# Kernel tuning notes

Measured on AMD Instinct MI355X. Metric: run time of the kernel, lower is better.

Reference implementation:

```python
import jax, jax.numpy as jnp
import numpy as np

NEG_SLOPE = 0.2

def symlog(v):
    return jnp.sign(v) * jnp.log1p(jnp.abs(v))

def conv1d(v, w, b):
    # v: (N, Cin, L), w: (Cout, Cin, 3), 'same' padding, stride 1
    out = jax.lax.conv_general_dilated(v, w, (1,), 'SAME',
                                       dimension_numbers=('NCH', 'OIH', 'NCH'))
    return out + b[None, :, None]

def glorot(key, shape, fan_in, fan_out):
    s = jnp.sqrt(6.0 / (fan_in + fan_out))
    return jax.random.uniform(key, shape, jnp.float32, -s, s)

def setup_inputs() -> dict:
    N, L, E = 20000, 128, 320000
    IN, H, C, OHC = 512, 8, 32, 8
    key = jax.random.key(0)
    ks = jax.random.split(key, 12)
    x = jax.random.normal(ks[0], (N, IN), jnp.float32)
    onehot = jax.random.uniform(ks[1], (N, L), jnp.float32)
    src = jax.random.randint(ks[2], (E,), 0, N)
    off = jax.random.randint(ks[3], (E,), 1, N)
    dst = (src + off) % N  # guarantees no self loops
    adj = jnp.stack([src, dst], axis=0).astype(jnp.int64)
    lin_w = glorot(ks[4], (IN + OHC, H * C), IN + OHC, H * C)
    att_l = glorot(ks[5], (1, H, C), C, C)
    att_r = glorot(ks[6], (1, H, C), C, C)
    bias = jnp.zeros((H * C,), jnp.float32)
    conv1_w = glorot(ks[7], (8, 1, 3), 3, 24)
    conv1_b = jnp.zeros((8,), jnp.float32)
    conv2_w = glorot(ks[8], (16, 8, 3), 24, 48)
    conv2_b = jnp.zeros((16,), jnp.float32)
    lin2_w = glorot(ks[9], (16, OHC), 16, OHC)
    lin2_b = jnp.zeros((OHC,), jnp.float32)
    return {"x": x, "onehot": onehot, "adj": adj, "n_nodes": N,
            "lin_w": lin_w, "att_l": att_l, "att_r": att_r, "bias": bias,
            "conv1_w": conv1_w, "conv1_b": conv1_b,
            "conv2_w": conv2_w, "conv2_b": conv2_b,
            "lin2_w": lin2_w, "lin2_b": lin2_b}

def reference(x, onehot, adj, n_nodes, lin_w, att_l, att_r, bias,
              conv1_w, conv1_b, conv2_w, conv2_b, lin2_w, lin2_b):
    N = n_nodes
    H, C = att_l.shape[1], att_l.shape[2]
    # one-hot conv pipe: sort -> symlog -> conv-relu x2 -> global avg pool -> linear
    prepared = symlog(jnp.sort(onehot, axis=-1))[:, None, :]  # (N,1,L)
    h = jax.nn.relu(conv1d(prepared, conv1_w, conv1_b))
    h = jax.nn.relu(conv1d(h, conv2_w, conv2_b))
    readout = h.mean(axis=-1) @ lin2_w + lin2_b  # (N, OHC)
    xin = jnp.concatenate([x, readout], axis=-1)
    xh = (xin @ lin_w).reshape(N, H, C)
    al = (xh * att_l).sum(axis=-1)  # (N,H) sending alphas
    ar = (xh * att_r).sum(axis=-1)  # (N,H) receiving alphas
    # add self loops (input adj has none, so remove_self_loops is a no-op)
    loops = jnp.arange(N, dtype=adj.dtype)
    src = jnp.concatenate([adj[0], loops])
    dst = jnp.concatenate([adj[1], loops])
    # GAT-style attention with segment softmax over receiving nodes
    alpha = jax.nn.leaky_relu(al[src] + ar[dst], NEG_SLOPE)  # (Etot,H)
    amax = jax.ops.segment_max(alpha, dst, num_segments=N)
    ex = jnp.exp(alpha - amax[dst])
    denom = jax.ops.segment_sum(ex, dst, num_segments=N)
    alpha = ex / denom[dst]
    # weight + scatter-add aggregate
    wx = xh[src] * alpha[..., None]  # (Etot,H,C)
    new_x = jax.ops.segment_sum(wx, dst, num_segments=N).reshape(N, H * C) + bias
    new_onehot = jax.ops.segment_sum(onehot[src], dst, num_segments=N) + onehot
    return new_x, new_onehot
```

## Files before the change

### kernel.cpp

```cpp
#include <hip/hip_runtime.h>

#define NEG_SLOPE 0.2f

typedef __attribute__((ext_vector_type(4))) float f32x4;
typedef __attribute__((ext_vector_type(2))) float f32x2;
typedef __attribute__((ext_vector_type(8))) short short8;

__device__ __forceinline__ f32x2 mk2(float a, float b) { f32x2 r; r[0] = a; r[1] = b; return r; }

__device__ __forceinline__ f32x2 FMA2(f32x2 a, f32x2 b, f32x2 c) {
#if __has_builtin(__builtin_elementwise_fma)
    return __builtin_elementwise_fma(a, b, c);
#else
    f32x2 r; r[0] = fmaf(a[0], b[0], c[0]); r[1] = fmaf(a[1], b[1], c[1]); return r;
#endif
}

__device__ __forceinline__ ushort f2bf(float f) {
    uint u = __float_as_uint(f);
    u += 0x7FFFu + ((u >> 16) & 1u);
    return (ushort)(u >> 16);
}
__device__ __forceinline__ float bflo(uint u) { return __uint_as_float(u << 16); }
__device__ __forceinline__ float bfhi(uint u) { return __uint_as_float(u & 0xffff0000u); }

__global__ __launch_bounds__(256) void k_zero_int(int* __restrict__ p, int n) {
    int i = blockIdx.x * 256 + threadIdx.x;
    if (i < n) p[i] = 0;
}

__global__ __launch_bounds__(256) void k_conv_wave(
    const float* __restrict__ onehot,
    const float* __restrict__ c1w, const float* __restrict__ c1b,
    const float* __restrict__ c2w, const float* __restrict__ c2b,
    const float* __restrict__ l2w, const float* __restrict__ l2b,
    float* __restrict__ readout, uint* __restrict__ ohb, int N) {
    const int wave = threadIdx.x >> 6;
    const int lane = threadIdx.x & 63;
    const int n = blockIdx.x * 4 + wave;
    if (n >= N) return;

    float2 in2 = *reinterpret_cast<const float2*>(&onehot[(size_t)n * 128 + lane * 2]);
    ohb[(size_t)n*64 + lane] = (uint)f2bf(in2.x) | ((uint)f2bf(in2.y) << 16);
    float v0 = log1pf(in2.x);
    float v1 = log1pf(in2.y);

    #pragma unroll
    for (int k = 2; k <= 128; k <<= 1) {
        const bool asc = ((lane & (k >> 1)) == 0);
        #pragma unroll
        for (int j = k >> 1; j >= 2; j >>= 1) {
            const int m = j >> 1;
            float p0 = __shfl_xor(v0, m, 64);
            float p1 = __shfl_xor(v1, m, 64);
            const bool keepmin = (((lane & m) == 0) == asc);
            v0 = keepmin ? fminf(v0, p0) : fmaxf(v0, p0);
            v1 = keepmin ? fminf(v1, p1) : fmaxf(v1, p1);
        }
        float lo = fminf(v0, v1), hi = fmaxf(v0, v1);
        v0 = asc ? lo : hi;
        v1 = asc ? hi : lo;
    }

    float pm = __shfl_up(v1, 1, 64); if (lane == 0)  pm = 0.f;
    float pp = __shfl_down(v0, 1, 64); if (lane == 63) pp = 0.f;

    float h0[8], h1[8];
    {
        const f32x2 xm = mk2(pm, v0), x0 = mk2(v0, v1), xp = mk2(v1, pp);
        #pragma unroll
        for (int c = 0; c < 8; ++c) {
            const float w0 = c1w[c*3+0], w1 = c1w[c*3+1], w2 = c1w[c*3+2], b = c1b[c];
            f32x2 h = FMA2(xm, mk2(w0, w0), FMA2(x0, mk2(w1, w1), FMA2(xp, mk2(w2, w2), mk2(b, b))));
            h0[c] = fmaxf(h[0], 0.f);
            h1[c] = fmaxf(h[1], 0.f);
        }
    }

    f32x2 a01[16];
    #pragma unroll
    for (int c = 0; c < 16; ++c) { float b = c2b[c]; a01[c] = mk2(b, b); }
    #pragma unroll
    for (int ci = 0; ci < 8; ++ci) {
        float hm = __shfl_up(h1[ci], 1, 64); if (lane == 0)  hm = 0.f;
        float hp = __shfl_down(h0[ci], 1, 64); if (lane == 63) hp = 0.f;
        const f32x2 xm = mk2(hm, h0[ci]), x0 = mk2(h0[ci], h1[ci]), xp = mk2(h1[ci], hp);
        #pragma unroll
        for (int c = 0; c < 16; ++c) {
            const float w0 = c2w[(c*8+ci)*3+0], w1 = c2w[(c*8+ci)*3+1], w2 = c2w[(c*8+ci)*3+2];
            a01[c] = FMA2(xm, mk2(w0, w0), FMA2(x0, mk2(w1, w1), FMA2(xp, mk2(w2, w2), a01[c])));
        }
    }

    float pv[16];
    #pragma unroll
    for (int c = 0; c < 16; ++c) pv[c] = fmaxf(a01[c][0], 0.f) + fmaxf(a01[c][1], 0.f);

    {
        const bool up1 = lane & 1;
        #pragma unroll
        for (int j = 0; j < 8; ++j) {
            float send = up1 ? pv[j] : pv[j+8];
            float keep = up1 ? pv[j+8] : pv[j];
            pv[j] = keep + __shfl_xor(send, 1, 64);
        }
        const bool up2 = (lane >> 1) & 1;
        #pragma unroll
        for (int j = 0; j < 4; ++j) {
            float send = up2 ? pv[j] : pv[j+4];
            float keep = up2 ? pv[j+4] : pv[j];
            pv[j] = keep + __shfl_xor(send, 2, 64);
        }
        const bool up3 = (lane >> 2) & 1;
        #pragma unroll
        for (int j = 0; j < 2; ++j) {
            float send = up3 ? pv[j] : pv[j+2];
            float keep = up3 ? pv[j+2] : pv[j];
            pv[j] = keep + __shfl_xor(send, 4, 64);
        }
        const bool up4 = (lane >> 3) & 1;
        {
            float send = up4 ? pv[0] : pv[1];
            float keep = up4 ? pv[1] : pv[0];
            pv[0] = keep + __shfl_xor(send, 8, 64);
        }
        pv[0] += __shfl_xor(pv[0], 16, 64);
        pv[0] += __shfl_xor(pv[0], 32, 64);
    }

    float pooled[16];
    #pragma unroll
    for (int c = 0; c < 16; ++c) {
        const int s = ((c & 1) << 3) | (((c >> 1) & 1) << 2) | (((c >> 2) & 1) << 1) | ((c >> 3) & 1);
        pooled[c] = __shfl(pv[0], s, 64);
    }
    if (lane < 8) {
        float r = l2b[lane];
        #pragma unroll
        for (int c = 0; c < 16; ++c) r = fmaf(pooled[c] * (1.f/128.f), l2w[c*8 + lane], r);
        readout[(size_t)n*8 + lane] = r;
    }
}

__global__ __launch_bounds__(256) void k_prepB(const float* __restrict__ lin_w, ushort* __restrict__ Bt) {
    const int col = blockIdx.x;
    for (int k = threadIdx.x; k < 544; k += 256) {
        float v = (k < 520) ? lin_w[(size_t)k*256 + col] : 0.f;
        Bt[(size_t)col*544 + k] = f2bf(v);
    }
}

__global__ __launch_bounds__(128) void k_gemm_mfma(
    const float* __restrict__ x, const float* __restrict__ readout,
    const ushort* __restrict__ Bt,
    const float* __restrict__ att_l, const float* __restrict__ att_r,
    float* __restrict__ xh, ushort* __restrict__ xhb,
    float* __restrict__ al, float* __restrict__ ar, int N) {
    __shared__ __align__(16) unsigned char smem[8704];
    ushort* sA = (ushort*)smem;
    ushort* sB = sA + 1024;
    float*  ep = (float*)smem;

    const int t = threadIdx.x;
    const int wv = t >> 6, lane = t & 63;
    const int m0 = (blockIdx.x >> 2) * 32;
    const int c0 = (blockIdx.x & 3) * 64;

    const int arow = m0 + ((t >> 6) << 4) + (t & 15);
    const int akg  = (t >> 4) & 3;
    const int bcol0 = c0 + ((t >> 6) << 4) + (t & 15);
    const int bcol1 = c0 + (((t >> 6) + 2) << 4) + (t & 15);
    const int bkg   = (t >> 4) & 3;

    const bool arow_ok = (arow < N);

    f32x4 acc[4];
    #pragma unroll
    for (int j = 0; j < 4; ++j) acc[j] = (f32x4)0.f;

    float av[8];
    uint4 bv0, bv1;

#define LOAD_STEP(K0_)                                                            \
    {                                                                             \
        const int kk = (K0_) + akg * 8;                                           \
        if (arow_ok && kk < 520) {                                                \
            const float* p = (kk < 512) ? &x[(size_t)arow*512 + kk]               \
                                        : &readout[(size_t)arow*8];               \
            float4 lo = *reinterpret_cast<const float4*>(p);                      \
            float4 hi = *reinterpret_cast<const float4*>(p + 4);                  \
            av[0]=lo.x; av[1]=lo.y; av[2]=lo.z; av[3]=lo.w;                       \
            av[4]=hi.x; av[5]=hi.y; av[6]=hi.z; av[7]=hi.w;                       \
        } else {                                                                  \
            av[0]=av[1]=av[2]=av[3]=av[4]=av[5]=av[6]=av[7]=0.f;                  \
        }                                                                         \
        bv0 = *reinterpret_cast<const uint4*>(&Bt[(size_t)bcol0*544 + (K0_) + bkg*8]); \
        bv1 = *reinterpret_cast<const uint4*>(&Bt[(size_t)bcol1*544 + (K0_) + bkg*8]); \
    }

    LOAD_STEP(0)
    for (int k0 = 0; k0 < 544; k0 += 32) {
        __syncthreads();
        uint4 aw;
        aw.x = (uint)f2bf(av[0]) | ((uint)f2bf(av[1]) << 16);
        aw.y = (uint)f2bf(av[2]) | ((uint)f2bf(av[3]) << 16);
        aw.z = (uint)f2bf(av[4]) | ((uint)f2bf(av[5]) << 16);
        aw.w = (uint)f2bf(av[6]) | ((uint)f2bf(av[7]) << 16);
        *reinterpret_cast<uint4*>(&sA[t*8]) = aw;
        *reinterpret_cast<uint4*>(&sB[t*8]) = bv0;
        *reinterpret_cast<uint4*>(&sB[(t+128)*8]) = bv1;
        if (k0 + 32 < 544) LOAD_STEP(k0 + 32)
        __syncthreads();
        short8 af = *reinterpret_cast<const short8*>(&sA[(wv*64 + lane)*8]);
        #pragma unroll
        for (int j = 0; j < 4; ++j) {
            short8 bf = *reinterpret_cast<const short8*>(&sB[(j*64 + lane)*8]);
            acc[j] = __builtin_amdgcn_mfma_f32_16x16x32_bf16(af, bf, acc[j], 0, 0, 0);
        }
    }
#undef LOAD_STEP

    __syncthreads();
    {
        const int rb = wv*16 + (lane >> 4)*4;
        const int cb = lane & 15;
        #pragma unroll
        for (int j = 0; j < 4; ++j)
            #pragma unroll
            for (int r = 0; r < 4; ++r)
                ep[(rb + r)*68 + j*16 + cb] = acc[j][r];
    }
    __syncthreads();
    {
        const int rl = t >> 2;
        const int cq = (t & 3) * 16;
        const int row = m0 + rl;
        if (row < N) {
            const float* s = &ep[rl*68 + cq];
            float vals[16];
            #pragma unroll
            for (int i = 0; i < 16; ++i) vals[i] = s[i];
            float* dst = &xh[(size_t)row*256 + c0 + cq];
            #pragma unroll
            for (int i = 0; i < 4; ++i)
                *reinterpret_cast<float4*>(&dst[4*i]) = make_float4(vals[4*i], vals[4*i+1], vals[4*i+2], vals[4*i+3]);
            uint u[8];
            #pragma unroll
            for (int i = 0; i < 8; ++i)
                u[i] = (uint)f2bf(vals[2*i]) | ((uint)f2bf(vals[2*i+1]) << 16);
            ushort* db = &xhb[(size_t)row*256 + c0 + cq];
            *reinterpret_cast<uint4*>(db)     = make_uint4(u[0], u[1], u[2], u[3]);
            *reinterpret_cast<uint4*>(db + 8) = make_uint4(u[4], u[5], u[6], u[7]);
            float pl = 0.f, pr = 0.f;
            #pragma unroll
            for (int i = 0; i < 16; ++i) {
                pl = fmaf(vals[i], att_l[c0 + cq + i], pl);
                pr = fmaf(vals[i], att_r[c0 + cq + i], pr);
            }
            pl += __shfl_xor(pl, 1, 64);
            pr += __shfl_xor(pr, 1, 64);
            if ((t & 1) == 0) {
                const int head = (c0 >> 5) + ((t & 3) >> 1);
                al[(size_t)row*8 + head] = pl;
                ar[(size_t)row*8 + head] = pr;
            }
        }
    }
}

__global__ __launch_bounds__(256) void k_deg(const int* __restrict__ dst, int* __restrict__ deg, int E) {
    int e = blockIdx.x * 256 + threadIdx.x;
    if (e < E) atomicAdd(&deg[dst[e]], 1);
}

__global__ __launch_bounds__(1024) void k_scan(const int* __restrict__ deg, int* __restrict__ row_start, int N) {
    __shared__ int wsum[16];
    __shared__ int carry;
    const int t = threadIdx.x;
    const int w = t >> 6, ln = t & 63;
    if (t == 0) { carry = 0; row_start[0] = 0; }
    __syncthreads();
    for (int start = 0; start < N; start += 1024) {
        int i = start + t;
        int v = (i < N) ? deg[i] : 0;
        int s = v;
        #pragma unroll
        for (int d = 1; d < 64; d <<= 1) {
            int u = __shfl_up(s, d, 64);
            if (ln >= d) s += u;
        }
        if (ln == 63) wsum[w] = s;
        __syncthreads();
        if (w == 0) {
            int ws = (ln < 16) ? wsum[ln] : 0;
            int e = ws;
            #pragma unroll
            for (int d = 1; d < 16; d <<= 1) {
                int u = __shfl_up(e, d, 64);
                if (ln >= d) e += u;
            }
            if (ln < 16) wsum[ln] = e - ws;
        }
        __syncthreads();
        int incl = s + wsum[w] + carry;
        if (i < N) row_start[i + 1] = incl;
        __syncthreads();
        if (t == 1023) carry = incl;
    }
}

__global__ __launch_bounds__(256) void k_fill(
    const int* __restrict__ src, const int* __restrict__ dst,
    const int* __restrict__ row_start, int* __restrict__ cursor,
    int* __restrict__ csr, int E) {
    int e = blockIdx.x * 256 + threadIdx.x;
    if (e < E) {
        int d = dst[e];
        int p = atomicAdd(&cursor[d], 1);
        csr[row_start[d] + p] = src[e];
    }
}

__global__ __launch_bounds__(256) void k_agg(
    const float* __restrict__ xh, const ushort* __restrict__ xhb,
    const float* __restrict__ al, const float* __restrict__ ar,
    const float* __restrict__ onehot, const uint* __restrict__ ohb,
    const float* __restrict__ bias,
    const int* __restrict__ row_start, const int* __restrict__ csr,
    float* __restrict__ out_x, float* __restrict__ out_oh, int N) {
    const int wave = threadIdx.x >> 6;
    const int lane = threadIdx.x & 63;
    const int n = blockIdx.x * 4 + wave;
    if (n >= N) return;
    const int h = lane >> 3;
    const float ard = ar[(size_t)n*8 + h];

    float a_self = al[(size_t)n*8 + h] + ard;
    a_self = (a_self > 0.f) ? a_self : NEG_SLOPE * a_self;
    float m = a_self;
    float den = 1.f;
    float4 acc = *reinterpret_cast<const float4*>(&xh[(size_t)n*256 + lane*4]);
    float oh0 = 0.f, oh1 = 0.f;

    const int beg = row_start[n], end = row_start[n+1];
    for (int i = beg; i < end; ++i) {
        int sidx = csr[i];
        float a = al[(size_t)sidx*8 + h] + ard;
        a = (a > 0.f) ? a : NEG_SLOPE * a;
        float mn = fmaxf(m, a);
        float scale = __expf(m - mn);
        float e = __expf(a - mn);
        m = mn;
        uint2 xb = *reinterpret_cast<const uint2*>(&xhb[(size_t)sidx*256 + lane*4]);
        acc.x = fmaf(e, bflo(xb.x), acc.x * scale);
        acc.y = fmaf(e, bfhi(xb.x), acc.y * scale);
        acc.z = fmaf(e, bflo(xb.y), acc.z * scale);
        acc.w = fmaf(e, bfhi(xb.y), acc.w * scale);
        den = den * scale + e;
        uint ob = ohb[(size_t)sidx*64 + lane];
        oh0 += bflo(ob); oh1 += bfhi(ob);
    }
    float inv = 1.f / den;
    const float4 bv = *reinterpret_cast<const float4*>(&bias[lane*4]);
    float4 o;
    o.x = fmaf(acc.x, inv, bv.x);
    o.y = fmaf(acc.y, inv, bv.y);
    o.z = fmaf(acc.z, inv, bv.z);
    o.w = fmaf(acc.w, inv, bv.w);
    *reinterpret_cast<float4*>(&out_x[(size_t)n*256 + lane*4]) = o;
    float2 so = *reinterpret_cast<const float2*>(&onehot[(size_t)n*128 + lane*2]);
    float2 oo;
    oo.x = oh0 + 2.f*so.x;
    oo.y = oh1 + 2.f*so.y;
    *reinterpret_cast<float2*>(&out_oh[(size_t)n*128 + lane*2]) = oo;
}

extern "C" void kernel_launch(void* const* d_in, const int* in_sizes, int n_in,
                              void* d_out, int out_size, void* d_ws, size_t ws_size,
                              hipStream_t stream) {
    const float* x      = (const float*)d_in[0];
    const float* onehot = (const float*)d_in[1];
    const int*   adj    = (const int*)d_in[2];
    const float* lin_w  = (const float*)d_in[4];
    const float* att_l  = (const float*)d_in[5];
    const float* att_r  = (const float*)d_in[6];
    const float* bias   = (const float*)d_in[7];
    const float* c1w    = (const float*)d_in[8];
    const float* c1b    = (const float*)d_in[9];
    const float* c2w    = (const float*)d_in[10];
    const float* c2b    = (const float*)d_in[11];
    const float* l2w    = (const float*)d_in[12];
    const float* l2b    = (const float*)d_in[13];

    const int N = in_sizes[0] / 512;
    const int E = in_sizes[2] / 2;
    const int* src = adj;
    const int* dst = adj + E;

    float* out_x  = (float*)d_out;
    float* out_oh = out_x + (size_t)N * 256;

    float* readout   = (float*)d_ws;
    float* xh        = readout + (size_t)N * 8;
    float* al        = xh + (size_t)N * 256;
    float* ar        = al + (size_t)N * 8;
    ushort* Bt       = (ushort*)(ar + (size_t)N * 8);
    ushort* xhb      = Bt + (size_t)256 * 544;
    uint*   ohb      = (uint*)(xhb + (size_t)N * 256);
    int*   row_start = (int*)(ohb + (size_t)N * 64);
    int*   cursor    = row_start + (N + 1);
    int*   csr       = cursor + N;

    const int EB = (E + 255) / 256;
    const int NB = (N + 255) / 256;

    k_zero_int<<<NB, 256, 0, stream>>>(cursor, N);
    k_conv_wave<<<(N + 3) / 4, 256, 0, stream>>>(onehot, c1w, c1b, c2w, c2b, l2w, l2b, readout, ohb, N);
    k_prepB<<<256, 256, 0, stream>>>(lin_w, Bt);
    k_deg<<<EB, 256, 0, stream>>>(dst, cursor, E);
    k_gemm_mfma<<<((N + 31) / 32) * 4, 128, 0, stream>>>(x, readout, Bt, att_l, att_r, xh, xhb, al, ar, N);
    k_scan<<<1, 1024, 0, stream>>>(cursor, row_start, N);
    k_zero_int<<<NB, 256, 0, stream>>>(cursor, N);
    k_fill<<<EB, 256, 0, stream>>>(src, dst, row_start, cursor, csr, E);
    k_agg<<<(N + 3) / 4, 256, 0, stream>>>(xh, xhb, al, ar, onehot, ohb, bias, row_start, csr, out_x, out_oh, N);
}
```

Measured before the change: 199.1 us.

## Drop online-softmax max tracking, unroll edge loop by two, fold cursor zeroing into scan

The aggregation kernel no longer keeps a running max with rescaling. It uses plain exp of the leaky-relu logits, which removes one exp and the rescale multiplies per edge and shortens the serial dependency chain. The edge loop is unrolled by two so more gathers are in flight at once. The scan kernel now zeroes the degree counters as it reads them, which removes one kernel launch. Dropping the max subtraction risks overflow for large logits, and it relies on the attention values staying small.

```diff
diff --git a/kernel.cpp b/kernel.cpp
--- a/kernel.cpp
+++ b/kernel.cpp
@@ -273,7 +273,7 @@
     if (e < E) atomicAdd(&deg[dst[e]], 1);
 }
 
-__global__ __launch_bounds__(1024) void k_scan(const int* __restrict__ deg, int* __restrict__ row_start, int N) {
+__global__ __launch_bounds__(1024) void k_scan(int* __restrict__ deg, int* __restrict__ row_start, int N) {
     __shared__ int wsum[16];
     __shared__ int carry;
     const int t = threadIdx.x;
@@ -282,7 +282,8 @@
     __syncthreads();
     for (int start = 0; start < N; start += 1024) {
         int i = start + t;
-        int v = (i < N) ? deg[i] : 0;
+        int v = 0;
+        if (i < N) { v = deg[i]; deg[i] = 0; }
         int s = v;
         #pragma unroll
         for (int d = 1; d < 64; d <<= 1) {
@@ -337,30 +338,49 @@
 
     float a_self = al[(size_t)n*8 + h] + ard;
     a_self = (a_self > 0.f) ? a_self : NEG_SLOPE * a_self;
-    float m = a_self;
-    float den = 1.f;
-    float4 acc = *reinterpret_cast<const float4*>(&xh[(size_t)n*256 + lane*4]);
+    float e_self = __expf(a_self);
+    float4 xs = *reinterpret_cast<const float4*>(&xh[(size_t)n*256 + lane*4]);
+    float4 acc;
+    acc.x = e_self * xs.x; acc.y = e_self * xs.y; acc.z = e_self * xs.z; acc.w = e_self * xs.w;
+    float den = e_self;
     float oh0 = 0.f, oh1 = 0.f;
 
     const int beg = row_start[n], end = row_start[n+1];
-    for (int i = beg; i < end; ++i) {
-        int sidx = csr[i];
-        float a = al[(size_t)sidx*8 + h] + ard;
-        a = (a > 0.f) ? a : NEG_SLOPE * a;
-        float mn = fmaxf(m, a);
-        float scale = __expf(m - mn);
-        float e = __expf(a - mn);
-        m = mn;
-        uint2 xb = *reinterpret_cast<const uint2*>(&xhb[(size_t)sidx*256 + lane*4]);
-        acc.x = fmaf(e, bflo(xb.x), acc.x * scale);
-        acc.y = fmaf(e, bfhi(xb.x), acc.y * scale);
-        acc.z = fmaf(e, bflo(xb.y), acc.z * scale);
-        acc.w = fmaf(e, bfhi(xb.y), acc.w * scale);
-        den = den * scale + e;
-        uint ob = ohb[(size_t)sidx*64 + lane];
-        oh0 += bflo(ob); oh1 += bfhi(ob);
-    }
-    float inv = 1.f / den;
+    int i = beg;
+    for (; i + 1 < end; i += 2) {
+        const int s0 = csr[i], s1 = csr[i+1];
+        const float al0 = al[(size_t)s0*8 + h], al1 = al[(size_t)s1*8 + h];
+        const uint2 xb0 = *reinterpret_cast<const uint2*>(&xhb[(size_t)s0*256 + lane*4]);
+        const uint2 xb1 = *reinterpret_cast<const uint2*>(&xhb[(size_t)s1*256 + lane*4]);
+        const uint ob0 = ohb[(size_t)s0*64 + lane];
+        const uint ob1 = ohb[(size_t)s1*64 + lane];
+        float a0 = al0 + ard; a0 = (a0 > 0.f) ? a0 : NEG_SLOPE * a0;
+        float a1 = al1 + ard; a1 = (a1 > 0.f) ? a1 : NEG_SLOPE * a1;
+        const float e0 = __expf(a0), e1 = __expf(a1);
+        acc.x = fmaf(e0, bflo(xb0.x), fmaf(e1, bflo(xb1.x), acc.x));
+        acc.y = fmaf(e0, bfhi(xb0.x), fmaf(e1, bfhi(xb1.x), acc.y));
+        acc.z = fmaf(e0, bflo(xb0.y), fmaf(e1, bflo(xb1.y), acc.z));
+        acc.w = fmaf(e0, bfhi(xb0.y), fmaf(e1, bfhi(xb1.y), acc.w));
+        den += e0 + e1;
+        oh0 += bflo(ob0) + bflo(ob1);
+        oh1 += bfhi(ob0) + bfhi(ob1);
+    }
+    if (i < end) {
+        const int s0 = csr[i];
+        float a0 = al[(size_t)s0*8 + h] + ard;
+        a0 = (a0 > 0.f) ? a0 : NEG_SLOPE * a0;
+        const float e0 = __expf(a0);
+        const uint2 xb0 = *reinterpret_cast<const uint2*>(&xhb[(size_t)s0*256 + lane*4]);
+        const uint ob0 = ohb[(size_t)s0*64 + lane];
+        acc.x = fmaf(e0, bflo(xb0.x), acc.x);
+        acc.y = fmaf(e0, bfhi(xb0.x), acc.y);
+        acc.z = fmaf(e0, bflo(xb0.y), acc.z);
+        acc.w = fmaf(e0, bfhi(xb0.y), acc.w);
+        den += e0;
+        oh0 += bflo(ob0);
+        oh1 += bfhi(ob0);
+    }
+    const float inv = 1.f / den;
     const float4 bv = *reinterpret_cast<const float4*>(&bias[lane*4]);
     float4 o;
     o.x = fmaf(acc.x, inv, bv.x);
@@ -420,7 +440,6 @@
     k_deg<<<EB, 256, 0, stream>>>(dst, cursor, E);
     k_gemm_mfma<<<((N + 31) / 32) * 4, 128, 0, stream>>>(x, readout, Bt, att_l, att_r, xh, xhb, al, ar, N);
     k_scan<<<1, 1024, 0, stream>>>(cursor, row_start, N);
-    k_zero_int<<<NB, 256, 0, stream>>>(cursor, N);
     k_fill<<<EB, 256, 0, stream>>>(src, dst, row_start, cursor, csr, E);
     k_agg<<<(N + 3) / 4, 256, 0, stream>>>(xh, xhb, al, ar, onehot, ohb, bias, row_start, csr, out_x, out_oh, N);
 }
```

New measurement: 187.4 us. 1.06x faster.
